# Kernel optimization log

Hardware: AMD Instinct MI355X
Metric: run time of the kernel (lower is better)

Reference implementation:

```python
import jax, jax.numpy as jnp
import numpy as np

EPS = 1e-6
D_CONV = 4

def _layernorm(x):
    m = jnp.mean(x, axis=-1, keepdims=True)
    v = jnp.mean((x - m) ** 2, axis=-1, keepdims=True)
    return (x - m) / jnp.sqrt(v + EPS)

def setup_inputs() -> dict:
    key = jax.random.key(0)
    ks = jax.random.split(key, 20)
    B, L, D = 2, 4096, 1024
    Di = D          # expand = 1
    N = 16          # d_state
    R = 64          # dt_rank = ceil(D/16)
    H = 4 * D       # mlp hidden
    s = 0.02
    rn = lambda k, sh: s * jax.random.normal(k, sh, dtype=jnp.float32)
    x = jax.random.normal(ks[0], (B, L, D), dtype=jnp.float32)
    path = jax.random.permutation(ks[1], L).astype(jnp.int32)
    path_rev = jnp.argsort(path).astype(jnp.int32)
    A_log = jnp.log(jnp.tile(jnp.arange(1, N + 1, dtype=jnp.float32)[None, :], (Di, 1)))
    return {
        'x': x, 'path': path, 'path_rev': path_rev,
        'in_proj_w': rn(ks[2], (2 * Di, D)),
        'conv_w': rn(ks[3], (Di, D_CONV)), 'conv_b': rn(ks[4], (Di,)),
        'x_proj_w': rn(ks[5], (R + 2 * N, Di)),
        'dt_proj_w': rn(ks[6], (Di, R)), 'dt_proj_b': rn(ks[7], (Di,)),
        'A_log': A_log, 'D_param': jnp.ones((Di,), dtype=jnp.float32),
        'out_proj_w': rn(ks[8], (D, Di)),
        'fc1_w': rn(ks[9], (H, D)), 'fc1_b': jnp.zeros((H,), dtype=jnp.float32),
        'fc2_w': rn(ks[10], (D, H)), 'fc2_b': jnp.zeros((D,), dtype=jnp.float32),
    }

def _mamba(u, in_proj_w, conv_w, conv_b, x_proj_w, dt_proj_w, dt_proj_b, A_log, D_param, out_proj_w):
    B, L, _ = u.shape
    N = A_log.shape[1]
    R = dt_proj_w.shape[1]
    xz = u @ in_proj_w.T                      # (B,L,2*Di)
    xi, z = jnp.split(xz, 2, axis=-1)
    # causal depthwise conv1d, kernel 4
    xpad = jnp.pad(xi, ((0, 0), (D_CONV - 1, 0), (0, 0)))
    xc = conv_b + sum(conv_w[:, k] * xpad[:, k:k + L, :] for k in range(D_CONV))
    xc = jax.nn.silu(xc)                      # (B,L,Di)
    proj = xc @ x_proj_w.T                    # (B,L,R+2N)
    dt_r = proj[..., :R]
    Bm = proj[..., R:R + N]                   # (B,L,N)
    Cm = proj[..., R + N:]                    # (B,L,N)
    dt = jax.nn.softplus(dt_r @ dt_proj_w.T + dt_proj_b)  # (B,L,Di)
    A = -jnp.exp(A_log)                       # (Di,N)

    def step(h, inp):
        dt_t, B_t, C_t, x_t = inp             # (B,Di),(B,N),(B,N),(B,Di)
        dA = jnp.exp(dt_t[:, :, None] * A)    # (B,Di,N)
        h = dA * h + (dt_t * x_t)[:, :, None] * B_t[:, None, :]
        y = jnp.einsum('bdn,bn->bd', h, C_t)
        return h, y

    h0 = jnp.zeros((B, xc.shape[-1], N), dtype=u.dtype)
    xs = (dt.transpose(1, 0, 2), Bm.transpose(1, 0, 2), Cm.transpose(1, 0, 2), xc.transpose(1, 0, 2))
    _, ys = jax.lax.scan(step, h0, xs)        # (L,B,Di)
    y = ys.transpose(1, 0, 2) + D_param * xc
    y = y * jax.nn.silu(z)
    return y @ out_proj_w.T

def reference(x, path, path_rev, in_proj_w, conv_w, conv_b, x_proj_w, dt_proj_w, dt_proj_b,
              A_log, D_param, out_proj_w, fc1_w, fc1_b, fc2_w, fc2_b):
    tmp1 = x[:, path, :]                      # zigzag gather
    tmp1 = _mamba(_layernorm(tmp1), in_proj_w, conv_w, conv_b, x_proj_w,
                  dt_proj_w, dt_proj_b, A_log, D_param, out_proj_w)
    x = x + tmp1[:, path_rev, :]              # zigzag scatter (inverse gather)
    h = _layernorm(x)
    h = jax.nn.gelu(h @ fc1_w.T + fc1_b, approximate=True) @ fc2_w.T + fc2_b
    return x + h
```

## Files before the change

kernel.cpp:

```cpp
#include <hip/hip_runtime.h>
#include <cstdint>
#include <cstddef>

typedef unsigned short u16;
typedef __bf16 bf16x8 __attribute__((ext_vector_type(8)));
typedef float f32x4 __attribute__((ext_vector_type(4)));

#define B_ 2
#define L_ 4096
#define D_ 1024
#define N_ 16
#define BL_ 8192
#define NC_ 64
#define LC_ 64

__device__ __forceinline__ float bf2f(u16 h) {
  union { unsigned int u; float f; } v; v.u = ((unsigned int)h) << 16; return v.f;
}
__device__ __forceinline__ u16 f2bf(float f) {
  union { float f; unsigned int u; } v; v.f = f;
  unsigned int r = v.u + 0x7FFFu + ((v.u >> 16) & 1u);
  return (u16)(r >> 16);
}
__device__ __forceinline__ float sigmoidf_(float x) { return 1.0f / (1.0f + __expf(-x)); }

#define WBF_TOT 11730944
__global__ __launch_bounds__(256) void cvt_w_k(
    const float* __restrict__ s0, const float* __restrict__ s1,
    const float* __restrict__ s2, const float* __restrict__ s3,
    const float* __restrict__ s4, const float* __restrict__ s5,
    u16* __restrict__ dst)
{
  int i = blockIdx.x * 256 + threadIdx.x;
  if (i >= WBF_TOT) return;
  float v;
  if (i < 2097152) v = s0[i];
  else if (i < 2228224) { int j = i - 2097152; v = (j < 98304) ? s1[j] : 0.0f; }
  else if (i < 2293760) v = s2[i - 2228224];
  else if (i < 3342336) v = s3[i - 2293760];
  else if (i < 7536640) v = s4[i - 3342336];
  else v = s5[i - 7536640];
  dst[i] = f2bf(v);
}

#define BK 32
enum { M_BF16 = 0, M_PROJ = 1, M_SOFTPLUS = 2, M_GELU = 3, M_BIASRES = 4,
       M_PART = 5, M_ATOMIC = 6 };

#define GLDS(gp, lp) __builtin_amdgcn_global_load_lds( \
    (const __attribute__((address_space(1))) void*)(gp), \
    (__attribute__((address_space(3))) void*)(lp), 16, 0, 0)

template<int MODE>
__device__ __forceinline__ void epi_store(
    float v, size_t row, int col, int Nn, size_t zoff,
    float* __restrict__ C, u16* __restrict__ C2,
    const float* __restrict__ bias, const u16* __restrict__ resid)
{
  if constexpr (MODE == M_BF16) {
    C2[row * Nn + col] = f2bf(v);
  } else if constexpr (MODE == M_PART) {
    C2[zoff + row * Nn + col] = f2bf(v);
  } else if constexpr (MODE == M_ATOMIC) {
    atomicAdd(&C[row * Nn + col], v);
  } else if constexpr (MODE == M_SOFTPLUS) {
    v += bias[col];
    v = (v > 20.0f) ? v : log1pf(__expf(v));
    C2[row * Nn + col] = f2bf(v);
  } else if constexpr (MODE == M_GELU) {
    v += bias[col];
    float a = 0.7978845608028654f * (v + 0.044715f * v * v * v);
    float t = 1.0f - 2.0f / (__expf(2.0f * a) + 1.0f);
    C2[row * Nn + col] = f2bf(0.5f * v * (1.0f + t));
  } else if constexpr (MODE == M_BIASRES) {
    C[row * Nn + col] = v + bias[col] + bf2f(resid[row * Nn + col]);
  }
}

#define BM 128
#define BN 128

template<int MODE, int SPAN, int ROWK>
__global__ __launch_bounds__(256) void gemm_bt(
    const u16* __restrict__ A, const u16* __restrict__ W,
    float* __restrict__ C, u16* __restrict__ C2,
    const float* __restrict__ bias, const u16* __restrict__ resid,
    int M, int N)
{
  __shared__ __align__(16) u16 As[3][BM * BK];
  __shared__ __align__(16) u16 Bs[3][BN * BK];

  const int id = blockIdx.x + gridDim.x * blockIdx.y;
  const int xcd = id & 7;
  const int qq = id >> 3;
  const int bandH = gridDim.y >> 3;
  const int xs = qq % gridDim.x;
  const int ys = xcd * bandH + qq / gridDim.x;
  const int bm = ys * BM;
  const int bn = xs * BN;
  const int koff = blockIdx.z * SPAN;

  const int tid = threadIdx.x;
  const int lane = tid & 63;
  const int wave = tid >> 6;
  const int wr = (wave >> 1) * 64;
  const int wc = (wave & 1) * 64;

  f32x4 acc[4][4];
#pragma unroll
  for (int i = 0; i < 4; ++i)
#pragma unroll
    for (int j = 0; j < 4; ++j)
#pragma unroll
      for (int r = 0; r < 4; ++r) acc[i][j][r] = 0.0f;

  const int r0 = tid >> 2;
  const int ke = (((tid & 3) ^ (r0 & 3)) << 3);
  const u16* Ab = A + (size_t)(bm + r0) * ROWK + koff + ke;
  const u16* Wb = W + (size_t)(bn + r0) * ROWK + koff + ke;
  constexpr size_t rstep = (size_t)64 * ROWK;

  auto issue = [&](int buf, int k0) {
    GLDS(Ab + k0, &As[buf][tid * 8]);
    GLDS(Ab + k0 + rstep, &As[buf][(tid + 256) * 8]);
    GLDS(Wb + k0, &Bs[buf][tid * 8]);
    GLDS(Wb + k0 + rstep, &Bs[buf][(tid + 256) * 8]);
  };

  issue(0, 0);
  if constexpr (BK < SPAN) issue(1, BK);

  const int mr = lane & 15;
  const int pos = (((lane >> 4) ^ (mr & 3)) << 3);
  constexpr int NIT = SPAN / BK;

  auto step = [&](int it) {
    if (it + 1 < NIT) asm volatile("s_waitcnt vmcnt(4)" ::: "memory");
    else              asm volatile("s_waitcnt vmcnt(0)" ::: "memory");
    asm volatile("s_barrier" ::: "memory");
    if (it + 2 < NIT) issue((it + 2) % 3, (it + 2) * BK);
    const int cur = it % 3;
    bf16x8 af[4], bfr[4];
#pragma unroll
    for (int i = 0; i < 4; ++i)
      af[i] = *(const bf16x8*)(&As[cur][(wr + i * 16 + mr) * BK + pos]);
#pragma unroll
    for (int j = 0; j < 4; ++j)
      bfr[j] = *(const bf16x8*)(&Bs[cur][(wc + j * 16 + mr) * BK + pos]);
#pragma unroll
    for (int i = 0; i < 4; ++i)
#pragma unroll
      for (int j = 0; j < 4; ++j)
        acc[i][j] = __builtin_amdgcn_mfma_f32_16x16x32_bf16(af[i], bfr[j], acc[i][j], 0, 0, 0);
  };

  if constexpr (NIT <= 32) {
#pragma unroll
    for (int it = 0; it < NIT; ++it) step(it);
  } else {
#pragma unroll 8
    for (int it = 0; it < NIT; ++it) step(it);
  }

  const size_t zoff = (size_t)blockIdx.z * (size_t)M * (size_t)N;
  const int mlo = (lane >> 4) << 2;
  const int nlo = lane & 15;
#pragma unroll
  for (int i = 0; i < 4; ++i) {
#pragma unroll
    for (int j = 0; j < 4; ++j) {
      int col = bn + wc + j * 16 + nlo;
      if (col < N) {
#pragma unroll
        for (int r = 0; r < 4; ++r) {
          size_t row = (size_t)(bm + wr + i * 16 + mlo + r);
          float v = acc[i][j][r];
          if constexpr (MODE == M_PROJ) {
            C[row * 96 + col] = v;
            if (col < 64) C2[(row << 6) + col] = f2bf(v);
          } else {
            epi_store<MODE>(v, row, col, N, zoff, C, C2, bias, resid);
          }
        }
      }
    }
  }
}

#define BM2 128
#define BN2 256

template<int MODE, int K>
__global__ __launch_bounds__(256, 2) void gemm_big(
    const u16* __restrict__ A, const u16* __restrict__ W,
    float* __restrict__ C, u16* __restrict__ C2,
    const float* __restrict__ bias, const u16* __restrict__ resid,
    int M, int N)
{
  __shared__ __align__(16) u16 As[3][BM2 * BK];
  __shared__ __align__(16) u16 Bs[3][BN2 * BK];

  const int id = blockIdx.x + gridDim.x * blockIdx.y;
  const int xcd = id & 7;
  const int qq = id >> 3;
  const int bandH = gridDim.y >> 3;
  const int xs = qq % gridDim.x;
  const int ys = xcd * bandH + qq / gridDim.x;
  const int bm = ys * BM2;
  const int bn = xs * BN2;

  const int tid = threadIdx.x;
  const int lane = tid & 63;
  const int wave = tid >> 6;
  const int wm = (wave >> 1) * 64;
  const int wn = (wave & 1) * 128;

  f32x4 acc[4][8];
#pragma unroll
  for (int i = 0; i < 4; ++i)
#pragma unroll
    for (int j = 0; j < 8; ++j)
#pragma unroll
      for (int r = 0; r < 4; ++r) acc[i][j][r] = 0.0f;

  const int r0 = tid >> 2;
  const int ke = (((tid & 3) ^ (r0 & 3)) << 3);
  const u16* Ab = A + (size_t)(bm + r0) * K + ke;
  const u16* Wb = W + (size_t)(bn + r0) * K + ke;
  constexpr size_t rstep = (size_t)64 * K;

  auto issue = [&](int buf, int k0) {
    GLDS(Ab + k0, &As[buf][tid * 8]);
    GLDS(Ab + k0 + rstep, &As[buf][(tid + 256) * 8]);
    GLDS(Wb + k0, &Bs[buf][tid * 8]);
    GLDS(Wb + k0 + rstep,     &Bs[buf][(tid + 256) * 8]);
    GLDS(Wb + k0 + 2 * rstep, &Bs[buf][(tid + 512) * 8]);
    GLDS(Wb + k0 + 3 * rstep, &Bs[buf][(tid + 768) * 8]);
  };

  issue(0, 0);
  issue(1, BK);

  const int mr = lane & 15;
  const int pos = (((lane >> 4) ^ (mr & 3)) << 3);
  constexpr int NIT = K / BK;

  auto step = [&](int it) {
    if (it + 1 < NIT) asm volatile("s_waitcnt vmcnt(6)" ::: "memory");
    else              asm volatile("s_waitcnt vmcnt(0)" ::: "memory");
    asm volatile("s_barrier" ::: "memory");
    if (it + 2 < NIT) issue((it + 2) % 3, (it + 2) * BK);
    const int cur = it % 3;
    bf16x8 af[4], bfr[8];
#pragma unroll
    for (int i = 0; i < 4; ++i)
      af[i] = *(const bf16x8*)(&As[cur][(wm + i * 16 + mr) * BK + pos]);
#pragma unroll
    for (int j = 0; j < 8; ++j)
      bfr[j] = *(const bf16x8*)(&Bs[cur][(wn + j * 16 + mr) * BK + pos]);
#pragma unroll
    for (int i = 0; i < 4; ++i)
#pragma unroll
      for (int j = 0; j < 8; ++j)
        acc[i][j] = __builtin_amdgcn_mfma_f32_16x16x32_bf16(af[i], bfr[j], acc[i][j], 0, 0, 0);
  };

#pragma unroll
  for (int it = 0; it < NIT; ++it) step(it);

  const int mlo = (lane >> 4) << 2;
  const int nlo = lane & 15;
#pragma unroll
  for (int i = 0; i < 4; ++i) {
#pragma unroll
    for (int j = 0; j < 8; ++j) {
      int col = bn + wn + j * 16 + nlo;
#pragma unroll
      for (int r = 0; r < 4; ++r) {
        size_t row = (size_t)(bm + wm + i * 16 + mlo + r);
        epi_store<MODE>(acc[i][j][r], row, col, N, 0, C, C2, bias, resid);
      }
    }
  }
}

__global__ __launch_bounds__(256) void combine_k(
    const u16* __restrict__ part, const float* __restrict__ bias,
    const u16* __restrict__ resid, float* __restrict__ out)
{
  int idx = blockIdx.x * 256 + threadIdx.x;
  int col = idx & 1023;
  out[idx] = bf2f(part[idx]) + bf2f(part[idx + 8388608]) + bias[col] + bf2f(resid[idx]);
}

__global__ __launch_bounds__(256) void extract_dtr_k(
    const float* __restrict__ proj, u16* __restrict__ dtr)
{
  int idx = blockIdx.x * 256 + threadIdx.x;
  int m = idx >> 6, r = idx & 63;
  dtr[idx] = f2bf(proj[m * 96 + r]);
}

__device__ __forceinline__ void blockReduce2(float& s, float& q) {
#pragma unroll
  for (int o = 32; o > 0; o >>= 1) { s += __shfl_down(s, o, 64); q += __shfl_down(q, o, 64); }
  __shared__ float red[2][4];
  int lane = threadIdx.x & 63, wave = threadIdx.x >> 6;
  if (lane == 0) { red[0][wave] = s; red[1][wave] = q; }
  __syncthreads();
  s = red[0][0] + red[0][1] + red[0][2] + red[0][3];
  q = red[1][0] + red[1][1] + red[1][2] + red[1][3];
}

__global__ __launch_bounds__(256) void ln_gather_k(
    const float* __restrict__ x, const int* __restrict__ path, u16* __restrict__ out)
{
  int b = blockIdx.x >> 12;
  int l = blockIdx.x & 4095;
  int src = path[l];
  const float* row = x + (((size_t)b * L_ + src) << 10);
  u16* orow = out + (((size_t)b * L_ + l) << 10);
  float v[4], s = 0.f, q = 0.f;
#pragma unroll
  for (int i = 0; i < 4; ++i) {
    v[i] = row[threadIdx.x + (i << 8)];
    s += v[i]; q += v[i] * v[i];
  }
  blockReduce2(s, q);
  float mean = s * (1.0f / 1024.0f);
  float var = q * (1.0f / 1024.0f) - mean * mean;
  float rstd = rsqrtf(var + 1e-6f);
#pragma unroll
  for (int i = 0; i < 4; ++i)
    orow[threadIdx.x + (i << 8)] = f2bf((v[i] - mean) * rstd);
}

__global__ __launch_bounds__(256) void ln_scatter_k(
    const float* __restrict__ x, const int* __restrict__ prev,
    const u16* __restrict__ mo, u16* __restrict__ xnew, u16* __restrict__ lnout)
{
  int b = blockIdx.x >> 12;
  int l = blockIdx.x & 4095;
  int pl = prev[l];
  const float* xr = x + (((size_t)b * L_ + l) << 10);
  const u16* mr_ = mo + (((size_t)b * L_ + pl) << 10);
  size_t base = ((size_t)blockIdx.x) << 10;
  float v[4], s = 0.f, q = 0.f;
#pragma unroll
  for (int i = 0; i < 4; ++i) {
    v[i] = xr[threadIdx.x + (i << 8)] + bf2f(mr_[threadIdx.x + (i << 8)]);
    s += v[i]; q += v[i] * v[i];
  }
  blockReduce2(s, q);
  float mean = s * (1.0f / 1024.0f);
  float var = q * (1.0f / 1024.0f) - mean * mean;
  float rstd = rsqrtf(var + 1e-6f);
#pragma unroll
  for (int i = 0; i < 4; ++i) {
    xnew[base + threadIdx.x + (i << 8)] = f2bf(v[i]);
    lnout[base + threadIdx.x + (i << 8)] = f2bf((v[i] - mean) * rstd);
  }
}

__global__ __launch_bounds__(256) void conv_silu_k(
    const u16* __restrict__ xz, const float* __restrict__ cw, const float* __restrict__ cb,
    u16* __restrict__ xc)
{
  int idx = blockIdx.x * 256 + threadIdx.x;
  int d = idx & 1023;
  int l = (idx >> 10) & 4095;
  int b = idx >> 22;
  float acc = cb[d];
#pragma unroll
  for (int k = 0; k < 4; ++k) {
    int ls = l + k - 3;
    if (ls >= 0)
      acc += cw[(d << 2) + k] * bf2f(xz[(((size_t)b * L_ + ls) << 11) + d]);
  }
  acc = acc * sigmoidf_(acc);
  xc[idx] = f2bf(acc);
}

__global__ __launch_bounds__(256) void scan_p1_k(
    const u16* __restrict__ dt, const u16* __restrict__ xc, const float* __restrict__ proj,
    const float* __restrict__ A_log, float* __restrict__ acum, float* __restrict__ hloc)
{
  int c = blockIdx.x & (NC_ - 1);
  int q = (blockIdx.x >> 6) & 3;
  int b = blockIdx.x >> 8;
  int d = (q << 8) + threadIdx.x;
  float Arow[N_];
#pragma unroll
  for (int n = 0; n < N_; ++n) Arow[n] = -__expf(A_log[(d << 4) + n]);
  float h[N_], ac[N_];
#pragma unroll
  for (int n = 0; n < N_; ++n) { h[n] = 0.0f; ac[n] = 1.0f; }
  int l0 = c << 6;
  for (int i = 0; i < LC_; ++i) {
    size_t rowb = (size_t)b * L_ + (l0 + i);
    float dtv = bf2f(dt[(rowb << 10) + d]);
    float xv = bf2f(xc[(rowb << 10) + d]);
    float dtx = dtv * xv;
    const float* Bp = proj + rowb * 96 + 64;
#pragma unroll
    for (int n = 0; n < N_; ++n) {
      float dA = __expf(dtv * Arow[n]);
      h[n] = dA * h[n] + dtx * Bp[n];
      ac[n] *= dA;
    }
  }
  size_t sb = ((((size_t)b << 10) + d) << 10) + (c << 4);
#pragma unroll
  for (int n = 0; n < N_; ++n) { acum[sb + n] = ac[n]; hloc[sb + n] = h[n]; }
}

__global__ __launch_bounds__(256) void scan_p2_k(
    const float* __restrict__ acum, const float* __restrict__ hloc, float* __restrict__ hin)
{
  int idx = blockIdx.x * 256 + threadIdx.x;
  int n = idx & 15;
  int dn = idx >> 4;
  size_t base = ((size_t)dn << 10) + n;
  float hs = 0.0f;
  for (int c = 0; c < NC_; ++c) {
    hin[base + (c << 4)] = hs;
    hs = acum[base + (c << 4)] * hs + hloc[base + (c << 4)];
  }
}

__global__ __launch_bounds__(256) void scan_p3_k(
    const u16* __restrict__ dt, const u16* __restrict__ xc, const float* __restrict__ proj,
    const float* __restrict__ A_log, const float* __restrict__ Dp, const float* __restrict__ hin,
    const u16* __restrict__ xz, u16* __restrict__ yg)
{
  int c = blockIdx.x & (NC_ - 1);
  int q = (blockIdx.x >> 6) & 3;
  int b = blockIdx.x >> 8;
  int d = (q << 8) + threadIdx.x;
  float Arow[N_];
#pragma unroll
  for (int n = 0; n < N_; ++n) Arow[n] = -__expf(A_log[(d << 4) + n]);
  float h[N_];
  size_t sb = ((((size_t)b << 10) + d) << 10) + (c << 4);
#pragma unroll
  for (int n = 0; n < N_; ++n) h[n] = hin[sb + n];
  float Dv = Dp[d];
  int l0 = c << 6;
  for (int i = 0; i < LC_; ++i) {
    size_t rowb = (size_t)b * L_ + (l0 + i);
    float dtv = bf2f(dt[(rowb << 10) + d]);
    float xv = bf2f(xc[(rowb << 10) + d]);
    float dtx = dtv * xv;
    const float* Bp = proj + rowb * 96 + 64;
    const float* Cp = proj + rowb * 96 + 80;
    float y = 0.0f;
#pragma unroll
    for (int n = 0; n < N_; ++n) {
      float dA = __expf(dtv * Arow[n]);
      h[n] = dA * h[n] + dtx * Bp[n];
      y += h[n] * Cp[n];
    }
    y += Dv * xv;
    float zv = bf2f(xz[(rowb << 11) + 1024 + d]);
    yg[(rowb << 10) + d] = f2bf(y * zv * sigmoidf_(zv));
  }
}

extern "C" void kernel_launch(void* const* d_in, const int* in_sizes, int n_in,
                              void* d_out, int out_size, void* d_ws, size_t ws_size,
                              hipStream_t stream)
{
  const float* x_in      = (const float*)d_in[0];
  const int*   path      = (const int*)d_in[1];
  const int*   path_rev  = (const int*)d_in[2];
  const float* in_proj_w = (const float*)d_in[3];
  const float* conv_w    = (const float*)d_in[4];
  const float* conv_b    = (const float*)d_in[5];
  const float* x_proj_w  = (const float*)d_in[6];
  const float* dt_proj_w = (const float*)d_in[7];
  const float* dt_proj_b = (const float*)d_in[8];
  const float* A_log     = (const float*)d_in[9];
  const float* Dp        = (const float*)d_in[10];
  const float* out_pw    = (const float*)d_in[11];
  const float* fc1_w     = (const float*)d_in[12];
  const float* fc1_b     = (const float*)d_in[13];
  const float* fc2_w     = (const float*)d_in[14];
  const float* fc2_b     = (const float*)d_in[15];
  float* out = (float*)d_out;

  char* w = (char*)d_ws;
  size_t off = 0;
  auto alloc = [&](size_t bytes) -> char* {
    char* p = w + off;
    off = (off + bytes + 255) & ~(size_t)255;
    return p;
  };
  u16*   wbf   = (u16*)  alloc((size_t)WBF_TOT * 2);
  u16*   ln_bf = (u16*)  alloc((size_t)BL_ * 1024 * 2);
  u16*   xz    = (u16*)  alloc((size_t)BL_ * 2048 * 2);
  u16*   xc    = (u16*)  alloc((size_t)BL_ * 1024 * 2);
  char*  pool0 = alloc(0);
  float* proj  = (float*)alloc((size_t)BL_ * 96 * 4);
  u16*   dtr   = (u16*)  alloc((size_t)BL_ * 64 * 2);
  u16*   dt    = (u16*)  alloc((size_t)BL_ * 1024 * 2);
  float* acum  = (float*)alloc((size_t)2 * 1024 * NC_ * 16 * 4);
  float* hloc  = (float*)alloc((size_t)2 * 1024 * NC_ * 16 * 4);
  float* hin   = (float*)alloc((size_t)2 * 1024 * NC_ * 16 * 4);
  u16*   yg    = (u16*)  alloc((size_t)BL_ * 1024 * 2);
  u16*   h1b   = (u16*)pool0;
  off = (size_t)(pool0 - w) + ((size_t)BL_ * 4096 * 2);
  u16*   xnew  = (u16*)  alloc((size_t)BL_ * 1024 * 2);
  u16*   fcp   = (u16*)  alloc((size_t)2 * BL_ * 1024 * 2);
  u16*   mo    = xz;

  const u16* w_inp = wbf;
  const u16* w_xp  = wbf + 2097152;
  const u16* w_dtp = wbf + 2228224;
  const u16* w_op  = wbf + 2293760;
  const u16* w_fc1 = wbf + 3342336;
  const u16* w_fc2 = wbf + 7536640;

  dim3 blk(256);
  cvt_w_k<<<WBF_TOT / 256, blk, 0, stream>>>(in_proj_w, x_proj_w, dt_proj_w, out_pw,
                                             fc1_w, fc2_w, wbf);
  ln_gather_k<<<BL_, blk, 0, stream>>>(x_in, path, ln_bf);
  gemm_big<M_BF16, 1024><<<dim3(8, 64), blk, 0, stream>>>(ln_bf, w_inp, nullptr, xz, nullptr, nullptr, 8192, 2048);
  conv_silu_k<<<(BL_ * 1024) / 256, blk, 0, stream>>>(xz, conv_w, conv_b, xc);
  hipMemsetAsync(proj, 0, (size_t)BL_ * 96 * 4, stream);
  gemm_bt<M_ATOMIC, 256, 1024><<<dim3(1, 64, 4), blk, 0, stream>>>(xc, w_xp, proj, nullptr, nullptr, nullptr, 8192, 96);
  extract_dtr_k<<<(BL_ * 64) / 256, blk, 0, stream>>>(proj, dtr);
  gemm_bt<M_SOFTPLUS, 64, 64><<<dim3(8, 64), blk, 0, stream>>>(dtr, w_dtp, nullptr, dt, dt_proj_b, nullptr, 8192, 1024);
  scan_p1_k<<<2 * 4 * NC_, blk, 0, stream>>>(dt, xc, proj, A_log, acum, hloc);
  scan_p2_k<<<(2 * 1024 * 16) / 256, blk, 0, stream>>>(acum, hloc, hin);
  scan_p3_k<<<2 * 4 * NC_, blk, 0, stream>>>(dt, xc, proj, A_log, Dp, hin, xz, yg);
  gemm_big<M_BF16, 1024><<<dim3(4, 64), blk, 0, stream>>>(yg, w_op, nullptr, mo, nullptr, nullptr, 8192, 1024);
  ln_scatter_k<<<BL_, blk, 0, stream>>>(x_in, path_rev, mo, xnew, ln_bf);
  gemm_big<M_GELU, 1024><<<dim3(16, 64), blk, 0, stream>>>(ln_bf, w_fc1, nullptr, h1b, fc1_b, nullptr, 8192, 4096);
  gemm_bt<M_PART, 2048, 4096><<<dim3(8, 64, 2), blk, 0, stream>>>(h1b, w_fc2, nullptr, fcp, nullptr, nullptr, 8192, 1024);
  combine_k<<<(BL_ * 1024) / 256, blk, 0, stream>>>(fcp, fc2_b, xnew, out);
}
```

Before: 631.0 us.

## Switch big GEMMs to 256x256 tiles with 512 threads and split-K

Replaces the 128x256 GEMM kernel with a 256x256, 512-thread kernel that supports split-K, and uses it for in_proj, out_proj, fc1 and fc2. out_proj now runs as a two-way split-K followed by a combine kernel. The x_proj GEMM drops its atomic split-K, memset and dtr-extract pass and uses a single-pass kernel that writes dt_r as bf16 directly. The larger tiles give more data reuse per block but cut the block count and raise register pressure. The out_proj split-K adds an extra combine pass.

```diff
diff --git a/kernel.cpp b/kernel.cpp
--- a/kernel.cpp
+++ b/kernel.cpp
@@ -45,7 +45,7 @@
 
 #define BK 32
 enum { M_BF16 = 0, M_PROJ = 1, M_SOFTPLUS = 2, M_GELU = 3, M_BIASRES = 4,
-       M_PART = 5, M_ATOMIC = 6 };
+       M_PART = 5 };
 
 #define GLDS(gp, lp) __builtin_amdgcn_global_load_lds( \
     (const __attribute__((address_space(1))) void*)(gp), \
@@ -61,8 +61,6 @@
     C2[row * Nn + col] = f2bf(v);
   } else if constexpr (MODE == M_PART) {
     C2[zoff + row * Nn + col] = f2bf(v);
-  } else if constexpr (MODE == M_ATOMIC) {
-    atomicAdd(&C[row * Nn + col], v);
   } else if constexpr (MODE == M_SOFTPLUS) {
     v += bias[col];
     v = (v > 20.0f) ? v : log1pf(__expf(v));
@@ -154,13 +152,8 @@
         acc[i][j] = __builtin_amdgcn_mfma_f32_16x16x32_bf16(af[i], bfr[j], acc[i][j], 0, 0, 0);
   };
 
-  if constexpr (NIT <= 32) {
-#pragma unroll
-    for (int it = 0; it < NIT; ++it) step(it);
-  } else {
-#pragma unroll 8
-    for (int it = 0; it < NIT; ++it) step(it);
-  }
+#pragma unroll
+  for (int it = 0; it < NIT; ++it) step(it);
 
   const size_t zoff = (size_t)blockIdx.z * (size_t)M * (size_t)N;
   const int mlo = (lane >> 4) << 2;
@@ -187,18 +180,18 @@
   }
 }
 
-#define BM2 128
-#define BN2 256
-
-template<int MODE, int K>
-__global__ __launch_bounds__(256, 2) void gemm_big(
+#define BMH 256
+#define BNH 256
+
+template<int MODE, int SPAN, int ROWK>
+__global__ __launch_bounds__(512) void gemm_hg(
     const u16* __restrict__ A, const u16* __restrict__ W,
     float* __restrict__ C, u16* __restrict__ C2,
     const float* __restrict__ bias, const u16* __restrict__ resid,
     int M, int N)
 {
-  __shared__ __align__(16) u16 As[3][BM2 * BK];
-  __shared__ __align__(16) u16 Bs[3][BN2 * BK];
+  __shared__ __align__(16) u16 As[3][BMH * BK];
+  __shared__ __align__(16) u16 Bs[3][BNH * BK];
 
   const int id = blockIdx.x + gridDim.x * blockIdx.y;
   const int xcd = id & 7;
@@ -206,79 +199,84 @@
   const int bandH = gridDim.y >> 3;
   const int xs = qq % gridDim.x;
   const int ys = xcd * bandH + qq / gridDim.x;
-  const int bm = ys * BM2;
-  const int bn = xs * BN2;
+  const int bm = ys * BMH;
+  const int bn = xs * BNH;
+  const int koff = blockIdx.z * SPAN;
 
   const int tid = threadIdx.x;
   const int lane = tid & 63;
   const int wave = tid >> 6;
-  const int wm = (wave >> 1) * 64;
-  const int wn = (wave & 1) * 128;
-
-  f32x4 acc[4][8];
-#pragma unroll
-  for (int i = 0; i < 4; ++i)
-#pragma unroll
-    for (int j = 0; j < 8; ++j)
+  const int wm = (wave >> 2) * 128;
+  const int wn = (wave & 3) * 64;
+
+  f32x4 acc[8][4];
+#pragma unroll
+  for (int i = 0; i < 8; ++i)
+#pragma unroll
+    for (int j = 0; j < 4; ++j)
 #pragma unroll
       for (int r = 0; r < 4; ++r) acc[i][j][r] = 0.0f;
 
   const int r0 = tid >> 2;
   const int ke = (((tid & 3) ^ (r0 & 3)) << 3);
-  const u16* Ab = A + (size_t)(bm + r0) * K + ke;
-  const u16* Wb = W + (size_t)(bn + r0) * K + ke;
-  constexpr size_t rstep = (size_t)64 * K;
+  const u16* Ab = A + (size_t)(bm + r0) * ROWK + koff + ke;
+  const u16* Wb = W + (size_t)(bn + r0) * ROWK + koff + ke;
+  constexpr size_t rstep = (size_t)128 * ROWK;
 
   auto issue = [&](int buf, int k0) {
     GLDS(Ab + k0, &As[buf][tid * 8]);
-    GLDS(Ab + k0 + rstep, &As[buf][(tid + 256) * 8]);
+    GLDS(Ab + k0 + rstep, &As[buf][(tid + 512) * 8]);
     GLDS(Wb + k0, &Bs[buf][tid * 8]);
-    GLDS(Wb + k0 + rstep,     &Bs[buf][(tid + 256) * 8]);
-    GLDS(Wb + k0 + 2 * rstep, &Bs[buf][(tid + 512) * 8]);
-    GLDS(Wb + k0 + 3 * rstep, &Bs[buf][(tid + 768) * 8]);
+    GLDS(Wb + k0 + rstep, &Bs[buf][(tid + 512) * 8]);
   };
 
   issue(0, 0);
-  issue(1, BK);
+  if constexpr (BK < SPAN) issue(1, BK);
 
   const int mr = lane & 15;
   const int pos = (((lane >> 4) ^ (mr & 3)) << 3);
-  constexpr int NIT = K / BK;
+  constexpr int NIT = SPAN / BK;
 
   auto step = [&](int it) {
-    if (it + 1 < NIT) asm volatile("s_waitcnt vmcnt(6)" ::: "memory");
+    if (it + 1 < NIT) asm volatile("s_waitcnt vmcnt(4)" ::: "memory");
     else              asm volatile("s_waitcnt vmcnt(0)" ::: "memory");
     asm volatile("s_barrier" ::: "memory");
     if (it + 2 < NIT) issue((it + 2) % 3, (it + 2) * BK);
     const int cur = it % 3;
-    bf16x8 af[4], bfr[8];
-#pragma unroll
-    for (int i = 0; i < 4; ++i)
+    bf16x8 af[8], bfr[4];
+#pragma unroll
+    for (int i = 0; i < 8; ++i)
       af[i] = *(const bf16x8*)(&As[cur][(wm + i * 16 + mr) * BK + pos]);
 #pragma unroll
-    for (int j = 0; j < 8; ++j)
+    for (int j = 0; j < 4; ++j)
       bfr[j] = *(const bf16x8*)(&Bs[cur][(wn + j * 16 + mr) * BK + pos]);
 #pragma unroll
-    for (int i = 0; i < 4; ++i)
-#pragma unroll
-      for (int j = 0; j < 8; ++j)
+    for (int i = 0; i < 8; ++i)
+#pragma unroll
+      for (int j = 0; j < 4; ++j)
         acc[i][j] = __builtin_amdgcn_mfma_f32_16x16x32_bf16(af[i], bfr[j], acc[i][j], 0, 0, 0);
   };
 
-#pragma unroll
-  for (int it = 0; it < NIT; ++it) step(it);
-
+  if constexpr (NIT <= 16) {
+#pragma unroll
+    for (int it = 0; it < NIT; ++it) step(it);
+  } else {
+#pragma unroll 4
+    for (int it = 0; it < NIT; ++it) step(it);
+  }
+
+  const size_t zoff = (size_t)blockIdx.z * (size_t)M * (size_t)N;
   const int mlo = (lane >> 4) << 2;
   const int nlo = lane & 15;
 #pragma unroll
-  for (int i = 0; i < 4; ++i) {
-#pragma unroll
-    for (int j = 0; j < 8; ++j) {
+  for (int i = 0; i < 8; ++i) {
+#pragma unroll
+    for (int j = 0; j < 4; ++j) {
       int col = bn + wn + j * 16 + nlo;
 #pragma unroll
       for (int r = 0; r < 4; ++r) {
         size_t row = (size_t)(bm + wm + i * 16 + mlo + r);
-        epi_store<MODE>(acc[i][j][r], row, col, N, 0, C, C2, bias, resid);
+        epi_store<MODE>(acc[i][j][r], row, col, N, zoff, C, C2, bias, resid);
       }
     }
   }
@@ -293,12 +291,11 @@
   out[idx] = bf2f(part[idx]) + bf2f(part[idx + 8388608]) + bias[col] + bf2f(resid[idx]);
 }
 
-__global__ __launch_bounds__(256) void extract_dtr_k(
-    const float* __restrict__ proj, u16* __restrict__ dtr)
+__global__ __launch_bounds__(256) void combine_op_k(
+    const u16* __restrict__ part, u16* __restrict__ mo)
 {
   int idx = blockIdx.x * 256 + threadIdx.x;
-  int m = idx >> 6, r = idx & 63;
-  dtr[idx] = f2bf(proj[m * 96 + r]);
+  mo[idx] = f2bf(bf2f(part[idx]) + bf2f(part[idx + 8388608]));
 }
 
 __device__ __forceinline__ void blockReduce2(float& s, float& q) {
@@ -520,22 +517,21 @@
   const u16* w_fc1 = wbf + 3342336;
   const u16* w_fc2 = wbf + 7536640;
 
-  dim3 blk(256);
+  dim3 blk(256), blk5(512);
   cvt_w_k<<<WBF_TOT / 256, blk, 0, stream>>>(in_proj_w, x_proj_w, dt_proj_w, out_pw,
                                              fc1_w, fc2_w, wbf);
   ln_gather_k<<<BL_, blk, 0, stream>>>(x_in, path, ln_bf);
-  gemm_big<M_BF16, 1024><<<dim3(8, 64), blk, 0, stream>>>(ln_bf, w_inp, nullptr, xz, nullptr, nullptr, 8192, 2048);
+  gemm_hg<M_BF16, 1024, 1024><<<dim3(8, 32), blk5, 0, stream>>>(ln_bf, w_inp, nullptr, xz, nullptr, nullptr, 8192, 2048);
   conv_silu_k<<<(BL_ * 1024) / 256, blk, 0, stream>>>(xz, conv_w, conv_b, xc);
-  hipMemsetAsync(proj, 0, (size_t)BL_ * 96 * 4, stream);
-  gemm_bt<M_ATOMIC, 256, 1024><<<dim3(1, 64, 4), blk, 0, stream>>>(xc, w_xp, proj, nullptr, nullptr, nullptr, 8192, 96);
-  extract_dtr_k<<<(BL_ * 64) / 256, blk, 0, stream>>>(proj, dtr);
+  gemm_bt<M_PROJ, 1024, 1024><<<dim3(1, 64), blk, 0, stream>>>(xc, w_xp, proj, dtr, nullptr, nullptr, 8192, 96);
   gemm_bt<M_SOFTPLUS, 64, 64><<<dim3(8, 64), blk, 0, stream>>>(dtr, w_dtp, nullptr, dt, dt_proj_b, nullptr, 8192, 1024);
   scan_p1_k<<<2 * 4 * NC_, blk, 0, stream>>>(dt, xc, proj, A_log, acum, hloc);
   scan_p2_k<<<(2 * 1024 * 16) / 256, blk, 0, stream>>>(acum, hloc, hin);
   scan_p3_k<<<2 * 4 * NC_, blk, 0, stream>>>(dt, xc, proj, A_log, Dp, hin, xz, yg);
-  gemm_big<M_BF16, 1024><<<dim3(4, 64), blk, 0, stream>>>(yg, w_op, nullptr, mo, nullptr, nullptr, 8192, 1024);
+  gemm_hg<M_PART, 512, 1024><<<dim3(4, 32, 2), blk5, 0, stream>>>(yg, w_op, nullptr, fcp, nullptr, nullptr, 8192, 1024);
+  combine_op_k<<<(BL_ * 1024) / 256, blk, 0, stream>>>(fcp, mo);
   ln_scatter_k<<<BL_, blk, 0, stream>>>(x_in, path_rev, mo, xnew, ln_bf);
-  gemm_big<M_GELU, 1024><<<dim3(16, 64), blk, 0, stream>>>(ln_bf, w_fc1, nullptr, h1b, fc1_b, nullptr, 8192, 4096);
-  gemm_bt<M_PART, 2048, 4096><<<dim3(8, 64, 2), blk, 0, stream>>>(h1b, w_fc2, nullptr, fcp, nullptr, nullptr, 8192, 1024);
+  gemm_hg<M_GELU, 1024, 1024><<<dim3(16, 32), blk5, 0, stream>>>(ln_bf, w_fc1, nullptr, h1b, fc1_b, nullptr, 8192, 4096);
+  gemm_hg<M_PART, 2048, 4096><<<dim3(4, 32, 2), blk5, 0, stream>>>(h1b, w_fc2, nullptr, fcp, nullptr, nullptr, 8192, 1024);
   combine_k<<<(BL_ * 1024) / 256, blk, 0, stream>>>(fcp, fc2_b, xnew, out);
 }
```

New measurement: 632.3 us. Within noise of the previous version (+0.2%).
